# Kernel optimization log

Measured on AMD Instinct MI355X. Metric: run time of the kernel, lower is better.

## Reference

```python
import jax, jax.numpy as jnp
import numpy as np

N, E, G, H = 50000, 800000, 2048, 128
DIS = 3  # dis_emb is None -> raw frac_diff (3 dims)
EIN = 2 * H + 6 + DIS  # 265


def _lin_init(key, fan_in, fan_out):
    lim = 1.0 / np.sqrt(fan_in)
    return jax.random.uniform(key, (fan_in, fan_out), jnp.float32, -lim, lim)


def setup_inputs() -> dict:
    key = jax.random.key(0)
    ks = jax.random.split(key, 12)
    node_features = jax.random.normal(ks[0], (N, H), jnp.float32)
    frac_coords = jax.random.uniform(ks[1], (N, 3), jnp.float32)
    lattices = jax.random.normal(ks[2], (G, 6), jnp.float32)
    frac_diff = jax.random.normal(ks[3], (E, 3), jnp.float32)
    edge_index = jax.random.randint(ks[4], (2, E), 0, N, jnp.int64 if jax.config.jax_enable_x64 else jnp.int32)
    edge2graph = jax.random.randint(ks[5], (E,), 0, G, edge_index.dtype)
    return dict(
        node_features=node_features,
        frac_coords=frac_coords,
        lattices=lattices,
        frac_diff=frac_diff,
        edge_index=edge_index,
        edge2graph=edge2graph,
        e_w1=_lin_init(ks[6], EIN, H), e_b1=jnp.zeros((H,), jnp.float32),
        e_w2=_lin_init(ks[7], H, H), e_b2=jnp.zeros((H,), jnp.float32),
        n_w1=_lin_init(ks[8], 2 * H, H), n_b1=jnp.zeros((H,), jnp.float32),
        n_w2=_lin_init(ks[9], H, H), n_b2=jnp.zeros((H,), jnp.float32),
    )


def reference(node_features, frac_coords, lattices, frac_diff, edge_index, edge2graph,
              e_w1, e_b1, e_w2, e_b2, n_w1, n_b1, n_w2, n_b2):
    n_nodes = node_features.shape[0]
    silu = jax.nn.silu
    # edge model: gather endpoints, concat with per-graph lattice + frac_diff
    hi = node_features[edge_index[0]]            # [E, H]
    hj = node_features[edge_index[1]]            # [E, H]
    lat = lattices[edge2graph]                   # [E, 6]
    edges_input = jnp.concatenate([hi, hj, lat, frac_diff], axis=1)  # [E, 265]
    e = silu(edges_input @ e_w1 + e_b1)
    edge_features = silu(e @ e_w2 + e_b2)        # [E, H]
    # scatter-mean aggregate onto source nodes
    seg = edge_index[0]
    agg_sum = jax.ops.segment_sum(edge_features, seg, num_segments=n_nodes)
    cnt = jax.ops.segment_sum(jnp.ones((edge_features.shape[0],), edge_features.dtype), seg, num_segments=n_nodes)
    agg = agg_sum / jnp.maximum(cnt, 1.0)[:, None]
    # node model + residual
    h = jnp.concatenate([node_features, agg], axis=1)  # [N, 2H]
    h = silu(h @ n_w1 + n_b1)
    node_output = silu(h @ n_w2 + n_b2)
    return node_features + node_output
```

## Files before the change

kernel.cpp:

```cpp
#include <hip/hip_runtime.h>

#define N_NODES 50000
#define N_EDGES 800000
#define HDIM 128
#define N_GRAPH 2048

typedef __bf16 bf16x8 __attribute__((ext_vector_type(8)));
typedef float f32x4 __attribute__((ext_vector_type(4)));

static __device__ __forceinline__ unsigned short f2bf(float f) {
    unsigned int u = __float_as_uint(f);
    u += 0x7fffu + ((u >> 16) & 1u);
    return (unsigned short)(u >> 16);
}
static __device__ __forceinline__ float bflo(unsigned int u) { return __uint_as_float(u << 16); }
static __device__ __forceinline__ float bfhi(unsigned int u) { return __uint_as_float(u & 0xFFFF0000u); }

static __device__ __forceinline__ float silu_f(float x) {
    float e = __builtin_amdgcn_exp2f(x * -1.44269504f);
    return x * __builtin_amdgcn_rcpf(1.0f + e);
}

#define PREP_BLOCKS 1408
#define HIST_BLOCKS 3125
__global__ void prep_hist_kernel(const float* __restrict__ ew1, const float* __restrict__ ew2,
                                 const float* __restrict__ nw1, const float* __restrict__ nw2,
                                 const float* __restrict__ eb1, const float* __restrict__ lattices,
                                 const int* __restrict__ eidx,
                                 unsigned short* __restrict__ W1aT, unsigned short* __restrict__ W1bT,
                                 unsigned short* __restrict__ W2t, unsigned short* __restrict__ N1t,
                                 unsigned short* __restrict__ N2t, unsigned short* __restrict__ Lb,
                                 int* __restrict__ buf) {
    const int bid = blockIdx.x;
    if (bid >= PREP_BLOCKS) {
        int e = (bid - PREP_BLOCKS) * 256 + threadIdx.x;
        if (e < N_EDGES) atomicAdd(&buf[eidx[e]], 1);
        return;
    }
    int i = bid * 256 + threadIdx.x;
    if (i < 16384) {
        int n = i >> 7, k = i & 127;
        W1aT[i] = f2bf(ew1[k * 128 + n]);
    } else if (i < 32768) {
        int j = i - 16384; int n = j >> 7, k = j & 127;
        W1bT[j] = f2bf(ew1[(128 + k) * 128 + n]);
    } else if (i < 49152) {
        int j = i - 32768; int n = j >> 7, k = j & 127;
        W2t[j] = f2bf(ew2[k * 128 + n]);
    } else if (i < 81920) {
        int j = i - 49152; int n = j >> 8, k = j & 255;
        N1t[j] = f2bf(nw1[k * 128 + n]);
    } else if (i < 98304) {
        int j = i - 81920; int n = j >> 7, k = j & 127;
        N2t[j] = f2bf(nw2[k * 128 + n]);
    } else if (i < 98304 + 262144) {
        int j = i - 98304; int g = j >> 7, c = j & 127;
        float s = eb1[c];
#pragma unroll
        for (int t = 0; t < 6; ++t) s += lattices[g * 6 + t] * ew1[(256 + t) * 128 + c];
        Lb[j] = f2bf(s);
    }
}

__global__ __launch_bounds__(1024) void scan_kernel(int* __restrict__ buf) {
    constexpr int CH = 12288;
    __shared__ int lds[CH];
    __shared__ int part[1024];
    __shared__ int carry_s;
    const int t = threadIdx.x;
    if (t == 0) carry_s = 0;
    __syncthreads();
#pragma unroll 1
    for (int base = 0; base < N_NODES; base += CH) {
#pragma unroll
        for (int k = 0; k < CH / 1024; ++k) {
            int f = k * 1024 + t;
            lds[f] = (base + f < N_NODES) ? buf[base + f] : 0;
        }
        __syncthreads();
        int loc[12];
        int s = 0;
#pragma unroll
        for (int i = 0; i < 12; ++i) { loc[i] = lds[t * 12 + i]; s += loc[i]; }
        part[t] = s;
        __syncthreads();
        for (int off = 1; off < 1024; off <<= 1) {
            int tmp = (t >= off) ? part[t - off] : 0;
            __syncthreads();
            part[t] += tmp;
            __syncthreads();
        }
        const int total = part[1023];
        int run = carry_s + part[t] - s;
#pragma unroll
        for (int i = 0; i < 12; ++i) { int tmp = loc[i]; lds[t * 12 + i] = run; run += tmp; }
        __syncthreads();
#pragma unroll
        for (int k = 0; k < CH / 1024; ++k) {
            int f = k * 1024 + t;
            if (base + f < N_NODES) buf[base + f] = lds[f];
        }
        __syncthreads();
        if (t == 0) carry_s += total;
        __syncthreads();
    }
}

#define PERM_BLOCKS2 3125
#define PQ_BLOCKS ((N_NODES + 63) / 64)
__global__ __launch_bounds__(256, 4) void perm_pq_kernel(
    const int* __restrict__ eidx, const int* __restrict__ e2g,
    const float* __restrict__ frac_diff, int* __restrict__ buf,
    unsigned short* __restrict__ perm_lo, unsigned char* __restrict__ perm_hi,
    uint4* __restrict__ rec, const int packed,
    const float* __restrict__ nf, const unsigned short* __restrict__ W1aT,
    const unsigned short* __restrict__ W1bT,
    unsigned short* __restrict__ P, unsigned short* __restrict__ Qm) {
    constexpr int SA = 136;
    __shared__ unsigned short sm[64 * SA];
    const int bid = blockIdx.x;
    const int tid = threadIdx.x;

    if (bid < PERM_BLOCKS2) {
        int e = bid * 256 + tid;
        if (e < N_EDGES) {
            int s = eidx[e];
            int pos = atomicAdd(&buf[s], 1);
            if (packed) {
                int d = eidx[N_EDGES + e];
                int g = e2g[e];
                unsigned int w0 = (unsigned int)s | ((unsigned int)d << 16);
                unsigned int w1 = (unsigned int)g | ((unsigned int)f2bf(frac_diff[3 * e]) << 16);
                unsigned int w2 = (unsigned int)f2bf(frac_diff[3 * e + 1]) |
                                  ((unsigned int)f2bf(frac_diff[3 * e + 2]) << 16);
                rec[pos] = make_uint4(w0, w1, w2, 0u);
            } else {
                perm_lo[pos] = (unsigned short)(e & 0xFFFF);
                perm_hi[pos] = (unsigned char)(e >> 16);
            }
        }
        return;
    }

    const int n0 = (bid - PERM_BLOCKS2) * 64;
    const int mrow = tid >> 2, q = tid & 3;
    {
        const int node = n0 + mrow;
        unsigned short* row = sm + mrow * SA + q * 32;
        if (node < N_NODES) {
            const float4* a4 = (const float4*)(nf + (size_t)node * HDIM) + q * 8;
#pragma unroll
            for (int j = 0; j < 8; ++j) {
                float4 v = a4[j];
                *(ushort4*)(row + 4 * j) = make_ushort4(f2bf(v.x), f2bf(v.y), f2bf(v.z), f2bf(v.w));
            }
        } else {
#pragma unroll
            for (int j = 0; j < 8; ++j) *(ushort4*)(row + 4 * j) = make_ushort4(0, 0, 0, 0);
        }
    }
    __syncthreads();

    const int wave = tid >> 6, lane = tid & 63;
    const int lr = lane & 15, kq = lane >> 4;
    f32x4 acca[8] = {}, accb[8] = {};
    const int arow = (wave * 16 + lr) * SA;
#pragma unroll
    for (int ks = 0; ks < 128; ks += 32) {
        bf16x8 a = *(const bf16x8*)(sm + arow + ks + kq * 8);
#pragma unroll
        for (int nt = 0; nt < 8; ++nt) {
            bf16x8 ba = *(const bf16x8*)(W1aT + (nt * 16 + lr) * 128 + ks + kq * 8);
            acca[nt] = __builtin_amdgcn_mfma_f32_16x16x32_bf16(a, ba, acca[nt], 0, 0, 0);
            bf16x8 bb = *(const bf16x8*)(W1bT + (nt * 16 + lr) * 128 + ks + kq * 8);
            accb[nt] = __builtin_amdgcn_mfma_f32_16x16x32_bf16(a, bb, accb[nt], 0, 0, 0);
        }
    }
    __syncthreads();

    const int node = n0 + mrow;
#pragma unroll
    for (int nt = 0; nt < 8; ++nt) {
        const int col = nt * 16 + lr;
#pragma unroll
        for (int r = 0; r < 4; ++r)
            sm[(wave * 16 + kq * 4 + r) * SA + col] = f2bf(acca[nt][r]);
    }
    __syncthreads();
    if (node < N_NODES) {
        uint4* dst = (uint4*)(P + (size_t)node * HDIM + q * 32);
        const uint4* srcp = (const uint4*)(sm + mrow * SA + q * 32);
#pragma unroll
        for (int j = 0; j < 4; ++j) dst[j] = srcp[j];
    }
    __syncthreads();
#pragma unroll
    for (int nt = 0; nt < 8; ++nt) {
        const int col = nt * 16 + lr;
#pragma unroll
        for (int r = 0; r < 4; ++r)
            sm[(wave * 16 + kq * 4 + r) * SA + col] = f2bf(accb[nt][r]);
    }
    __syncthreads();
    if (node < N_NODES) {
        uint4* dst = (uint4*)(Qm + (size_t)node * HDIM + q * 32);
        const uint4* srcp = (const uint4*)(sm + mrow * SA + q * 32);
#pragma unroll
        for (int j = 0; j < 4; ++j) dst[j] = srcp[j];
    }
}

template <bool PACKED>
__global__ __launch_bounds__(256, 2) void edge_kernel(
    const unsigned short* __restrict__ P, const unsigned short* __restrict__ Qm,
    const unsigned short* __restrict__ Lb, const float* __restrict__ frac_diff,
    const int* __restrict__ eidx, const int* __restrict__ e2g,
    const unsigned short* __restrict__ perm_lo, const unsigned char* __restrict__ perm_hi,
    const uint4* __restrict__ rec,
    const float* __restrict__ e_w1, const unsigned short* __restrict__ W2t,
    const float* __restrict__ b2, float* __restrict__ agg) {
    const int tid = threadIdx.x;
    const int wv = tid >> 6, lane = tid & 63;
    const int lr = lane & 15, kq = lane >> 4;
    const int base = blockIdx.x * 64 + wv * 16;

    int src, dst, g;
    float fd0, fd1, fd2;
    if (PACKED) {
        const uint4 rv = rec[base + lr];
        src = rv.x & 0xFFFF;
        dst = rv.x >> 16;
        g = rv.y & 0xFFFF;
        fd0 = bfhi(rv.y);
        fd1 = bflo(rv.z);
        fd2 = bfhi(rv.z);
    } else {
        const int i = base + lr;
        const int e = (int)perm_lo[i] | ((int)perm_hi[i] << 16);
        src = eidx[e];
        dst = eidx[N_EDGES + e];
        g = e2g[e];
        fd0 = frac_diff[3 * e];
        fd1 = frac_diff[3 * e + 1];
        fd2 = frac_diff[3 * e + 2];
    }

    int sc[4], sn[4];
#pragma unroll
    for (int r = 0; r < 4; ++r) {
        const int row = kq * 4 + r;
        sc[r] = __shfl(src, row);
        sn[r] = __shfl(src, (row + 1) & 15);
    }

    const float* wrbase = e_w1 + 262 * HDIM;
    bf16x8 afrag[4];
#pragma unroll
    for (int ks = 0; ks < 4; ++ks) {
        const int c0 = ks * 32 + kq * 8;
        uint4 pu = *(const uint4*)(P + (size_t)src * HDIM + c0);
        uint4 qu = *(const uint4*)(Qm + (size_t)dst * HDIM + c0);
        uint4 lu = *(const uint4*)(Lb + (size_t)g * HDIM + c0);
        float w0[8], w1[8], w2[8];
        *(float4*)(w0) = *(const float4*)(wrbase + c0);
        *(float4*)(w0 + 4) = *(const float4*)(wrbase + c0 + 4);
        *(float4*)(w1) = *(const float4*)(wrbase + 128 + c0);
        *(float4*)(w1 + 4) = *(const float4*)(wrbase + 128 + c0 + 4);
        *(float4*)(w2) = *(const float4*)(wrbase + 256 + c0);
        *(float4*)(w2 + 4) = *(const float4*)(wrbase + 256 + c0 + 4);
        const unsigned int* pw = (const unsigned int*)&pu;
        const unsigned int* qw = (const unsigned int*)&qu;
        const unsigned int* lw = (const unsigned int*)&lu;
        unsigned int ow[4];
#pragma unroll
        for (int w = 0; w < 4; ++w) {
            float x0 = bflo(pw[w]) + bflo(qw[w]) + bflo(lw[w])
                     + fd0 * w0[2 * w] + fd1 * w1[2 * w] + fd2 * w2[2 * w];
            float x1 = bfhi(pw[w]) + bfhi(qw[w]) + bfhi(lw[w])
                     + fd0 * w0[2 * w + 1] + fd1 * w1[2 * w + 1] + fd2 * w2[2 * w + 1];
            ow[w] = (unsigned int)f2bf(silu_f(x0)) | ((unsigned int)f2bf(silu_f(x1)) << 16);
        }
        afrag[ks] = *(bf16x8*)ow;
    }

    f32x4 acc[8] = {};
#pragma unroll
    for (int ks = 0; ks < 4; ++ks) {
#pragma unroll
        for (int nt = 0; nt < 8; ++nt) {
            bf16x8 bb = *(const bf16x8*)(W2t + (nt * 16 + lr) * 128 + ks * 32 + kq * 8);
            acc[nt] = __builtin_amdgcn_mfma_f32_16x16x32_bf16(afrag[ks], bb, acc[nt], 0, 0, 0);
        }
    }

#pragma unroll
    for (int nt = 0; nt < 8; ++nt) {
        const int col = nt * 16 + lr;
        const float bias = b2[col];
        float p0 = silu_f(acc[nt][0] + bias);
        float p1 = p0 + silu_f(acc[nt][1] + bias);
        float p2 = p1 + silu_f(acc[nt][2] + bias);
        float p3 = p2 + silu_f(acc[nt][3] + bias);
        float t1 = __shfl_up(p3, 16);
        float t2 = __shfl_up(p3, 32);
        float t3 = __shfl_up(p3, 48);
        float off = 0.0f;
        if (kq > 0) off += t1;
        if (kq > 1) off += t2;
        if (kq > 2) off += t3;
        float pr[4] = { p0 + off, p1 + off, p2 + off, p3 + off };
#pragma unroll
        for (int r = 0; r < 4; ++r) {
            const int row = kq * 4 + r;
            const bool last = (row == 15);
            const bool bnd = last || (sc[r] != sn[r]);
            if (bnd) {
                atomicAdd(&agg[(size_t)sc[r] * HDIM + col], pr[r]);
                if (!last) atomicAdd(&agg[(size_t)sn[r] * HDIM + col], -pr[r]);
            }
        }
    }
}

__global__ __launch_bounds__(256, 4) void node_kernel(
    const float* __restrict__ nf, const float* __restrict__ agg,
    const int* __restrict__ buf,
    const unsigned short* __restrict__ N1t, const float* __restrict__ b1,
    const unsigned short* __restrict__ N2t, const float* __restrict__ b2,
    float* __restrict__ out) {
    constexpr int SA = 264;
    constexpr int S2 = 136;
    constexpr int SFo = 132;
    __shared__ unsigned short sm[64 * SA];
    float* smf = (float*)sm;

    const int tid = threadIdx.x;
    const int n0 = blockIdx.x * 64;
    const int mrow = tid >> 2, q = tid & 3;
    {
        const int node = n0 + mrow;
        unsigned short* row = sm + mrow * SA;
        const int cbq = q * 32;
        if (node < N_NODES) {
            const int c = buf[node] - (node ? buf[node - 1] : 0);
            const float inv = 1.0f / (float)max(c, 1);
            const float4* a4 = (const float4*)(nf + (size_t)node * HDIM) + q * 8;
            const float4* g4 = (const float4*)(agg + (size_t)node * HDIM) + q * 8;
#pragma unroll
            for (int j = 0; j < 8; ++j) {
                float4 v = a4[j];
                *(ushort4*)(row + cbq + 4 * j) =
                    make_ushort4(f2bf(v.x), f2bf(v.y), f2bf(v.z), f2bf(v.w));
                float4 g = g4[j];
                *(ushort4*)(row + HDIM + cbq + 4 * j) =
                    make_ushort4(f2bf(g.x * inv), f2bf(g.y * inv), f2bf(g.z * inv), f2bf(g.w * inv));
            }
        } else {
#pragma unroll
            for (int j = 0; j < 8; ++j) {
                *(ushort4*)(row + cbq + 4 * j) = make_ushort4(0, 0, 0, 0);
                *(ushort4*)(row + HDIM + cbq + 4 * j) = make_ushort4(0, 0, 0, 0);
            }
        }
    }
    __syncthreads();

    const int wave = tid >> 6, lane = tid & 63;
    const int lr = lane & 15, kq = lane >> 4;

    f32x4 acc[8] = {};
    const int arow = (wave * 16 + lr) * SA;
#pragma unroll
    for (int ks = 0; ks < 256; ks += 32) {
        bf16x8 a = *(const bf16x8*)(sm + arow + ks + kq * 8);
#pragma unroll
        for (int nt = 0; nt < 8; ++nt) {
            bf16x8 bb = *(const bf16x8*)(N1t + (nt * 16 + lr) * 256 + ks + kq * 8);
            acc[nt] = __builtin_amdgcn_mfma_f32_16x16x32_bf16(a, bb, acc[nt], 0, 0, 0);
        }
    }
    __syncthreads();

#pragma unroll
    for (int nt = 0; nt < 8; ++nt) {
        const int col = nt * 16 + lr;
        const float bias = b1[col];
#pragma unroll
        for (int r = 0; r < 4; ++r) {
            const int mm = wave * 16 + kq * 4 + r;
            sm[mm * S2 + col] = f2bf(silu_f(acc[nt][r] + bias));
        }
    }
    __syncthreads();

    f32x4 acc2[8] = {};
    const int arow2 = (wave * 16 + lr) * S2;
#pragma unroll
    for (int ks = 0; ks < 128; ks += 32) {
        bf16x8 a = *(const bf16x8*)(sm + arow2 + ks + kq * 8);
#pragma unroll
        for (int nt = 0; nt < 8; ++nt) {
            bf16x8 bb = *(const bf16x8*)(N2t + (nt * 16 + lr) * 128 + ks + kq * 8);
            acc2[nt] = __builtin_amdgcn_mfma_f32_16x16x32_bf16(a, bb, acc2[nt], 0, 0, 0);
        }
    }
    __syncthreads();

#pragma unroll
    for (int nt = 0; nt < 8; ++nt) {
        const int col = nt * 16 + lr;
        const float bias = b2[col];
#pragma unroll
        for (int r = 0; r < 4; ++r) {
            const int mm = wave * 16 + kq * 4 + r;
            smf[mm * SFo + col] = silu_f(acc2[nt][r] + bias);
        }
    }
    __syncthreads();
    {
        const int node = n0 + mrow;
        if (node < N_NODES) {
            const float4* nfr = (const float4*)(nf + (size_t)node * HDIM) + q * 8;
            float4* outr = (float4*)(out + (size_t)node * HDIM) + q * 8;
            const float* st = smf + mrow * SFo + q * 32;
#pragma unroll
            for (int j = 0; j < 8; ++j) {
                float4 v = nfr[j];
                float4 s4 = *(const float4*)(st + 4 * j);
                v.x += s4.x; v.y += s4.y; v.z += s4.z; v.w += s4.w;
                outr[j] = v;
            }
        }
    }
}

extern "C" void kernel_launch(void* const* d_in, const int* in_sizes, int n_in,
                              void* d_out, int out_size, void* d_ws, size_t ws_size,
                              hipStream_t stream) {
    const float* node_features = (const float*)d_in[0];
    const float* lattices = (const float*)d_in[2];
    const float* frac_diff = (const float*)d_in[3];
    const int* edge_index = (const int*)d_in[4];
    const int* edge2graph = (const int*)d_in[5];
    const float* e_w1 = (const float*)d_in[6];
    const float* e_b1 = (const float*)d_in[7];
    const float* e_w2 = (const float*)d_in[8];
    const float* e_b2 = (const float*)d_in[9];
    const float* n_w1 = (const float*)d_in[10];
    const float* n_b1 = (const float*)d_in[11];
    const float* n_w2 = (const float*)d_in[12];
    const float* n_b2 = (const float*)d_in[13];

    char* ws = (char*)d_ws;
    unsigned short* W1aT = (unsigned short*)(ws);
    unsigned short* W1bT = (unsigned short*)(ws + 32768);
    unsigned short* W2t  = (unsigned short*)(ws + 65536);
    unsigned short* N1t  = (unsigned short*)(ws + 98304);
    unsigned short* N2t  = (unsigned short*)(ws + 163840);
    unsigned short* Lb   = (unsigned short*)(ws + 196608);
    unsigned short* P    = (unsigned short*)(ws + 720896);
    unsigned short* Qm   = (unsigned short*)(ws + 13520896);
    int* buf             = (int*)(ws + 26320896);
    unsigned short* perm_lo = (unsigned short*)(ws + 26520896);
    unsigned char* perm_hi  = (unsigned char*)(ws + 28120896);
    uint4* rec           = (uint4*)(ws + 28920896);
    float* agg = (float*)d_out;

    const int packed = (ws_size >= 28920896 + (size_t)N_EDGES * 16) ? 1 : 0;

    hipMemsetAsync(d_out, 0, (size_t)N_NODES * HDIM * 4, stream);
    hipMemsetAsync(buf, 0, (size_t)N_NODES * 4, stream);

    prep_hist_kernel<<<PREP_BLOCKS + HIST_BLOCKS, 256, 0, stream>>>(
        e_w1, e_w2, n_w1, n_w2, e_b1, lattices, edge_index,
        W1aT, W1bT, W2t, N1t, N2t, Lb, buf);

    scan_kernel<<<1, 1024, 0, stream>>>(buf);

    perm_pq_kernel<<<PERM_BLOCKS2 + PQ_BLOCKS, 256, 0, stream>>>(
        edge_index, edge2graph, frac_diff, buf, perm_lo, perm_hi, rec, packed,
        node_features, W1aT, W1bT, P, Qm);

    if (packed) {
        edge_kernel<true><<<N_EDGES / 64, 256, 0, stream>>>(
            P, Qm, Lb, frac_diff, edge_index, edge2graph, perm_lo, perm_hi, rec,
            e_w1, W2t, e_b2, agg);
    } else {
        edge_kernel<false><<<N_EDGES / 64, 256, 0, stream>>>(
            P, Qm, Lb, frac_diff, edge_index, edge2graph, perm_lo, perm_hi, rec,
            e_w1, W2t, e_b2, agg);
    }

    node_kernel<<<(N_NODES + 63) / 64, 256, 0, stream>>>(
        node_features, agg, buf, N1t, n_b1, N2t, n_b2, (float*)d_out);
}
```

Before: 589.6 us.

## Software-pipeline edge kernel over multiple edge groups per wave and fuse agg zeroing

Each wave in the edge kernel now handles 5 consecutive 16-edge groups, prefetching the gathered P/Q/lattice rows for the next group and the metadata two groups ahead, so gather latency overlaps MFMA and atomic work. The frac_diff weight rows are packed to bf16 in LDS once per block, bf16 packing uses the hardware pack instruction, and the launch bound rises to 3 blocks. The memset of the aggregation buffer is folded into the prep kernel as extra blocks. This costs more registers for the prefetch buffers, and the frac weights are now rounded to bf16.

```diff
diff --git a/kernel.cpp b/kernel.cpp
--- a/kernel.cpp
+++ b/kernel.cpp
@@ -16,6 +16,12 @@
 static __device__ __forceinline__ float bflo(unsigned int u) { return __uint_as_float(u << 16); }
 static __device__ __forceinline__ float bfhi(unsigned int u) { return __uint_as_float(u & 0xFFFF0000u); }
 
+static __device__ __forceinline__ unsigned int cvt_pk_bf16(float lo, float hi) {
+    unsigned int r;
+    asm("v_cvt_pk_bf16_f32 %0, %1, %2" : "=v"(r) : "v"(lo), "v"(hi));
+    return r;
+}
+
 static __device__ __forceinline__ float silu_f(float x) {
     float e = __builtin_amdgcn_exp2f(x * -1.44269504f);
     return x * __builtin_amdgcn_rcpf(1.0f + e);
@@ -23,6 +29,7 @@
 
 #define PREP_BLOCKS 1408
 #define HIST_BLOCKS 3125
+#define ZERO_BLOCKS 6250
 __global__ void prep_hist_kernel(const float* __restrict__ ew1, const float* __restrict__ ew2,
                                  const float* __restrict__ nw1, const float* __restrict__ nw2,
                                  const float* __restrict__ eb1, const float* __restrict__ lattices,
@@ -30,8 +37,13 @@
                                  unsigned short* __restrict__ W1aT, unsigned short* __restrict__ W1bT,
                                  unsigned short* __restrict__ W2t, unsigned short* __restrict__ N1t,
                                  unsigned short* __restrict__ N2t, unsigned short* __restrict__ Lb,
-                                 int* __restrict__ buf) {
+                                 int* __restrict__ buf, float* __restrict__ agg) {
     const int bid = blockIdx.x;
+    if (bid >= PREP_BLOCKS + HIST_BLOCKS) {
+        const int idx = (bid - PREP_BLOCKS - HIST_BLOCKS) * 256 + threadIdx.x;
+        ((float4*)agg)[idx] = make_float4(0.f, 0.f, 0.f, 0.f);
+        return;
+    }
     if (bid >= PREP_BLOCKS) {
         int e = (bid - PREP_BLOCKS) * 256 + threadIdx.x;
         if (e < N_EDGES) atomicAdd(&buf[eidx[e]], 1);
@@ -210,8 +222,36 @@
     }
 }
 
+#define NG 5
+#define EDGE_BLOCKS (N_EDGES / (64 * NG))
+
 template <bool PACKED>
-__global__ __launch_bounds__(256, 2) void edge_kernel(
+static __device__ __forceinline__ void fetch_meta(
+    int i, const uint4* __restrict__ rec, const int* __restrict__ eidx,
+    const int* __restrict__ e2g, const float* __restrict__ frac_diff,
+    const unsigned short* __restrict__ perm_lo, const unsigned char* __restrict__ perm_hi,
+    int& src, int& dst, int& g, float& f0, float& f1, float& f2) {
+    if (PACKED) {
+        const uint4 rv = rec[i];
+        src = rv.x & 0xFFFF;
+        dst = rv.x >> 16;
+        g = rv.y & 0xFFFF;
+        f0 = bfhi(rv.y);
+        f1 = bflo(rv.z);
+        f2 = bfhi(rv.z);
+    } else {
+        const int e = (int)perm_lo[i] | ((int)perm_hi[i] << 16);
+        src = eidx[e];
+        dst = eidx[N_EDGES + e];
+        g = e2g[e];
+        f0 = frac_diff[3 * e];
+        f1 = frac_diff[3 * e + 1];
+        f2 = frac_diff[3 * e + 2];
+    }
+}
+
+template <bool PACKED>
+__global__ __launch_bounds__(256, 3) void edge_kernel(
     const unsigned short* __restrict__ P, const unsigned short* __restrict__ Qm,
     const unsigned short* __restrict__ Lb, const float* __restrict__ frac_diff,
     const int* __restrict__ eidx, const int* __restrict__ e2g,
@@ -219,106 +259,132 @@
     const uint4* __restrict__ rec,
     const float* __restrict__ e_w1, const unsigned short* __restrict__ W2t,
     const float* __restrict__ b2, float* __restrict__ agg) {
+
+    __shared__ __align__(16) unsigned int wlds[192];
     const int tid = threadIdx.x;
+    const float* wrbase = e_w1 + 262 * HDIM;
+    if (tid < 192) {
+        const int w = tid & 3, rw = (tid >> 2) % 3, ksv = (tid / 12) & 3, kqi = tid / 48;
+        const int c = ksv * 32 + kqi * 8 + 2 * w;
+        wlds[tid] = (unsigned int)f2bf(wrbase[rw * HDIM + c]) |
+                    ((unsigned int)f2bf(wrbase[rw * HDIM + c + 1]) << 16);
+    }
+    __syncthreads();
+
     const int wv = tid >> 6, lane = tid & 63;
     const int lr = lane & 15, kq = lane >> 4;
-    const int base = blockIdx.x * 64 + wv * 16;
-
-    int src, dst, g;
-    float fd0, fd1, fd2;
-    if (PACKED) {
-        const uint4 rv = rec[base + lr];
-        src = rv.x & 0xFFFF;
-        dst = rv.x >> 16;
-        g = rv.y & 0xFFFF;
-        fd0 = bfhi(rv.y);
-        fd1 = bflo(rv.z);
-        fd2 = bfhi(rv.z);
-    } else {
-        const int i = base + lr;
-        const int e = (int)perm_lo[i] | ((int)perm_hi[i] << 16);
-        src = eidx[e];
-        dst = eidx[N_EDGES + e];
-        g = e2g[e];
-        fd0 = frac_diff[3 * e];
-        fd1 = frac_diff[3 * e + 1];
-        fd2 = frac_diff[3 * e + 2];
-    }
-
-    int sc[4], sn[4];
-#pragma unroll
-    for (int r = 0; r < 4; ++r) {
-        const int row = kq * 4 + r;
-        sc[r] = __shfl(src, row);
-        sn[r] = __shfl(src, (row + 1) & 15);
-    }
-
-    const float* wrbase = e_w1 + 262 * HDIM;
-    bf16x8 afrag[4];
+    const int ebase = (blockIdx.x * 4 + wv) * (16 * NG);
+
+    int srcC, dstC, gC; float f0C, f1C, f2C;
+    fetch_meta<PACKED>(ebase + lr, rec, eidx, e2g, frac_diff, perm_lo, perm_hi,
+                       srcC, dstC, gC, f0C, f1C, f2C);
+    uint4 pu[4], qu[4], lu[4];
 #pragma unroll
     for (int ks = 0; ks < 4; ++ks) {
         const int c0 = ks * 32 + kq * 8;
-        uint4 pu = *(const uint4*)(P + (size_t)src * HDIM + c0);
-        uint4 qu = *(const uint4*)(Qm + (size_t)dst * HDIM + c0);
-        uint4 lu = *(const uint4*)(Lb + (size_t)g * HDIM + c0);
-        float w0[8], w1[8], w2[8];
-        *(float4*)(w0) = *(const float4*)(wrbase + c0);
-        *(float4*)(w0 + 4) = *(const float4*)(wrbase + c0 + 4);
-        *(float4*)(w1) = *(const float4*)(wrbase + 128 + c0);
-        *(float4*)(w1 + 4) = *(const float4*)(wrbase + 128 + c0 + 4);
-        *(float4*)(w2) = *(const float4*)(wrbase + 256 + c0);
-        *(float4*)(w2 + 4) = *(const float4*)(wrbase + 256 + c0 + 4);
-        const unsigned int* pw = (const unsigned int*)&pu;
-        const unsigned int* qw = (const unsigned int*)&qu;
-        const unsigned int* lw = (const unsigned int*)&lu;
-        unsigned int ow[4];
-#pragma unroll
-        for (int w = 0; w < 4; ++w) {
-            float x0 = bflo(pw[w]) + bflo(qw[w]) + bflo(lw[w])
-                     + fd0 * w0[2 * w] + fd1 * w1[2 * w] + fd2 * w2[2 * w];
-            float x1 = bfhi(pw[w]) + bfhi(qw[w]) + bfhi(lw[w])
-                     + fd0 * w0[2 * w + 1] + fd1 * w1[2 * w + 1] + fd2 * w2[2 * w + 1];
-            ow[w] = (unsigned int)f2bf(silu_f(x0)) | ((unsigned int)f2bf(silu_f(x1)) << 16);
-        }
-        afrag[ks] = *(bf16x8*)ow;
-    }
-
-    f32x4 acc[8] = {};
-#pragma unroll
-    for (int ks = 0; ks < 4; ++ks) {
-#pragma unroll
-        for (int nt = 0; nt < 8; ++nt) {
-            bf16x8 bb = *(const bf16x8*)(W2t + (nt * 16 + lr) * 128 + ks * 32 + kq * 8);
-            acc[nt] = __builtin_amdgcn_mfma_f32_16x16x32_bf16(afrag[ks], bb, acc[nt], 0, 0, 0);
-        }
-    }
-
-#pragma unroll
-    for (int nt = 0; nt < 8; ++nt) {
-        const int col = nt * 16 + lr;
-        const float bias = b2[col];
-        float p0 = silu_f(acc[nt][0] + bias);
-        float p1 = p0 + silu_f(acc[nt][1] + bias);
-        float p2 = p1 + silu_f(acc[nt][2] + bias);
-        float p3 = p2 + silu_f(acc[nt][3] + bias);
-        float t1 = __shfl_up(p3, 16);
-        float t2 = __shfl_up(p3, 32);
-        float t3 = __shfl_up(p3, 48);
-        float off = 0.0f;
-        if (kq > 0) off += t1;
-        if (kq > 1) off += t2;
-        if (kq > 2) off += t3;
-        float pr[4] = { p0 + off, p1 + off, p2 + off, p3 + off };
+        pu[ks] = *(const uint4*)(P + (size_t)srcC * HDIM + c0);
+        qu[ks] = *(const uint4*)(Qm + (size_t)dstC * HDIM + c0);
+        lu[ks] = *(const uint4*)(Lb + (size_t)gC * HDIM + c0);
+    }
+    int srcN, dstN, gN; float f0N, f1N, f2N;
+    fetch_meta<PACKED>(ebase + 16 + lr, rec, eidx, e2g, frac_diff, perm_lo, perm_hi,
+                       srcN, dstN, gN, f0N, f1N, f2N);
+
+#pragma unroll 1
+    for (int t = 0; t < NG; ++t) {
+        uint4 puN[4], quN[4], luN[4];
+#pragma unroll
+        for (int ks = 0; ks < 4; ++ks) {
+            const int c0 = ks * 32 + kq * 8;
+            puN[ks] = *(const uint4*)(P + (size_t)srcN * HDIM + c0);
+            quN[ks] = *(const uint4*)(Qm + (size_t)dstN * HDIM + c0);
+            luN[ks] = *(const uint4*)(Lb + (size_t)gN * HDIM + c0);
+        }
+        int srcNN, dstNN, gNN; float f0NN, f1NN, f2NN;
+        {
+            const int tnn = (t + 2 < NG) ? (t + 2) : t;
+            fetch_meta<PACKED>(ebase + tnn * 16 + lr, rec, eidx, e2g, frac_diff,
+                               perm_lo, perm_hi, srcNN, dstNN, gNN, f0NN, f1NN, f2NN);
+        }
+
+        int sc[4], sn[4];
 #pragma unroll
         for (int r = 0; r < 4; ++r) {
             const int row = kq * 4 + r;
-            const bool last = (row == 15);
-            const bool bnd = last || (sc[r] != sn[r]);
-            if (bnd) {
-                atomicAdd(&agg[(size_t)sc[r] * HDIM + col], pr[r]);
-                if (!last) atomicAdd(&agg[(size_t)sn[r] * HDIM + col], -pr[r]);
-            }
-        }
+            sc[r] = __shfl(srcC, row);
+            sn[r] = __shfl(srcC, (row + 1) & 15);
+        }
+
+        bf16x8 afrag[4];
+#pragma unroll
+        for (int ks = 0; ks < 4; ++ks) {
+            int wb = kq * 48 + ks * 12;
+            asm volatile("" : "+v"(wb));
+            const uint4 w0v = *(const uint4*)(wlds + wb);
+            const uint4 w1v = *(const uint4*)(wlds + wb + 4);
+            const uint4 w2v = *(const uint4*)(wlds + wb + 8);
+            const unsigned int* pw = (const unsigned int*)&pu[ks];
+            const unsigned int* qw = (const unsigned int*)&qu[ks];
+            const unsigned int* lw = (const unsigned int*)&lu[ks];
+            const unsigned int* w0w = (const unsigned int*)&w0v;
+            const unsigned int* w1w = (const unsigned int*)&w1v;
+            const unsigned int* w2w = (const unsigned int*)&w2v;
+            unsigned int ow[4];
+#pragma unroll
+            for (int w = 0; w < 4; ++w) {
+                float x0 = bflo(pw[w]) + bflo(qw[w]) + bflo(lw[w])
+                         + f0C * bflo(w0w[w]) + f1C * bflo(w1w[w]) + f2C * bflo(w2w[w]);
+                float x1 = bfhi(pw[w]) + bfhi(qw[w]) + bfhi(lw[w])
+                         + f0C * bfhi(w0w[w]) + f1C * bfhi(w1w[w]) + f2C * bfhi(w2w[w]);
+                ow[w] = cvt_pk_bf16(silu_f(x0), silu_f(x1));
+            }
+            afrag[ks] = *(bf16x8*)ow;
+        }
+
+        f32x4 acc[8] = {};
+        int zoff = 0;
+        asm volatile("" : "+v"(zoff));
+#pragma unroll
+        for (int ks = 0; ks < 4; ++ks) {
+#pragma unroll
+            for (int nt = 0; nt < 8; ++nt) {
+                bf16x8 bb = *(const bf16x8*)(W2t + zoff + (nt * 16 + lr) * 128 + ks * 32 + kq * 8);
+                acc[nt] = __builtin_amdgcn_mfma_f32_16x16x32_bf16(afrag[ks], bb, acc[nt], 0, 0, 0);
+            }
+        }
+
+#pragma unroll
+        for (int nt = 0; nt < 8; ++nt) {
+            const int col = nt * 16 + lr;
+            const float bias = b2[col];
+            float p0 = silu_f(acc[nt][0] + bias);
+            float p1 = p0 + silu_f(acc[nt][1] + bias);
+            float p2 = p1 + silu_f(acc[nt][2] + bias);
+            float p3 = p2 + silu_f(acc[nt][3] + bias);
+            float t1 = __shfl_up(p3, 16);
+            float t2 = __shfl_up(p3, 32);
+            float t3 = __shfl_up(p3, 48);
+            float off = 0.0f;
+            if (kq > 0) off += t1;
+            if (kq > 1) off += t2;
+            if (kq > 2) off += t3;
+            float pr[4] = { p0 + off, p1 + off, p2 + off, p3 + off };
+#pragma unroll
+            for (int r = 0; r < 4; ++r) {
+                const int row = kq * 4 + r;
+                const bool last = (row == 15);
+                const bool bnd = last || (sc[r] != sn[r]);
+                if (bnd) {
+                    atomicAdd(&agg[(size_t)sc[r] * HDIM + col], pr[r]);
+                    if (!last) atomicAdd(&agg[(size_t)sn[r] * HDIM + col], -pr[r]);
+                }
+            }
+        }
+
+#pragma unroll
+        for (int ks = 0; ks < 4; ++ks) { pu[ks] = puN[ks]; qu[ks] = quN[ks]; lu[ks] = luN[ks]; }
+        srcC = srcN; dstC = dstN; gC = gN; f0C = f0N; f1C = f1N; f2C = f2N;
+        srcN = srcNN; dstN = dstNN; gN = gNN; f0N = f0NN; f1N = f1NN; f2N = f2NN;
     }
 }
 
@@ -468,12 +534,11 @@
 
     const int packed = (ws_size >= 28920896 + (size_t)N_EDGES * 16) ? 1 : 0;
 
-    hipMemsetAsync(d_out, 0, (size_t)N_NODES * HDIM * 4, stream);
     hipMemsetAsync(buf, 0, (size_t)N_NODES * 4, stream);
 
-    prep_hist_kernel<<<PREP_BLOCKS + HIST_BLOCKS, 256, 0, stream>>>(
+    prep_hist_kernel<<<PREP_BLOCKS + HIST_BLOCKS + ZERO_BLOCKS, 256, 0, stream>>>(
         e_w1, e_w2, n_w1, n_w2, e_b1, lattices, edge_index,
-        W1aT, W1bT, W2t, N1t, N2t, Lb, buf);
+        W1aT, W1bT, W2t, N1t, N2t, Lb, buf, agg);
 
     scan_kernel<<<1, 1024, 0, stream>>>(buf);
 
@@ -482,11 +547,11 @@
         node_features, W1aT, W1bT, P, Qm);
 
     if (packed) {
-        edge_kernel<true><<<N_EDGES / 64, 256, 0, stream>>>(
+        edge_kernel<true><<<EDGE_BLOCKS, 256, 0, stream>>>(
             P, Qm, Lb, frac_diff, edge_index, edge2graph, perm_lo, perm_hi, rec,
             e_w1, W2t, e_b2, agg);
     } else {
-        edge_kernel<false><<<N_EDGES / 64, 256, 0, stream>>>(
+        edge_kernel<false><<<EDGE_BLOCKS, 256, 0, stream>>>(
             P, Qm, Lb, frac_diff, edge_index, edge2graph, perm_lo, perm_hi, rec,
             e_w1, W2t, e_b2, agg);
     }
```

After: 655.5 us. 11.2% more time.
